# Performance work log

Measured on AMD Instinct MI355X. Metric: run time of the kernel, lower is better.

## Reference

```python
import jax, jax.numpy as jnp
import numpy as np

CAPSULES = 64
CAPSULE_DIM = 32
ROUTINGS = 3
EPS = 1e-7  # K.epsilon()


def setup_inputs() -> dict:
    key = jax.random.key(0)
    k1, k2 = jax.random.split(key)
    inputs = jax.random.normal(k1, (32, 2048, 16), dtype=jnp.float32)
    # W: (capsules, input_capsules, capsule_dim, input_capsule_dim), glorot-ish scale
    W = jax.random.normal(k2, (CAPSULES, 2048, CAPSULE_DIM, 16), dtype=jnp.float32) * 0.05
    return {"inputs": inputs, "W": W}


def squash(s):
    # s: [..., capsule_dim]
    s_norm = jnp.sum(jnp.square(s), axis=-1, keepdims=True)
    scale = s_norm / (1.0 + s_norm) / jnp.sqrt(s_norm + EPS)
    return s * scale


def reference(inputs, W):
    # inputs: [b, i, j] (batch, input_capsules, input_capsule_dim)
    # W:      [c, i, d, j] (capsules, input_capsules, capsule_dim, input_capsule_dim)
    # u_hat = batched predictions: [b, c, i, d]
    u_hat = jnp.einsum('bij,cidj->bcid', inputs, W)
    B = inputs.shape[0]
    b = jnp.zeros((B, CAPSULES, u_hat.shape[2]), dtype=u_hat.dtype)
    v = None
    for r in range(ROUTINGS):
        c = jax.nn.softmax(b, axis=1)              # softmax over capsules axis
        s = jnp.einsum('bci,bcid->bcd', c, u_hat)  # weighted sum over input capsules
        v = squash(s)                              # [b, c, d]
        # Original updates b for r > 0; the update at the final iteration has no
        # effect on the output, so it is skipped for efficiency (identical math).
        if 0 < r < ROUTINGS - 1:
            b = b + jnp.einsum('bcd,bcid->bci', v, u_hat)
    return v
```

## Files before the change

### kernel.cpp

```cpp
#include <hip/hip_runtime.h>
#include <math.h>

#define B_   32
#define I_   2048
#define J_   16
#define C_   64
#define D_   32
#define CD_  2048
#define W_CSTR (I_*D_*J_)
#define W_ISTR (D_*J_)
#define X_BSTR (I_*J_)
#define EPS_ 1e-7f

typedef _Float16 half8 __attribute__((ext_vector_type(8)));
typedef float    f32x16 __attribute__((ext_vector_type(16)));


__device__ __forceinline__ half8 wfrag_from_f32(const float* __restrict__ W,
                                                int c, int i, int l) {
  const float* wp = W + (size_t)c*W_CSTR + (size_t)i*W_ISTR
                      + (size_t)(l & 31)*J_ + ((l >> 5) << 3);
  float4 a = *(const float4*)wp;
  float4 b = *(const float4*)(wp + 4);
  half8 h;
  h[0]=(_Float16)a.x; h[1]=(_Float16)a.y; h[2]=(_Float16)a.z; h[3]=(_Float16)a.w;
  h[4]=(_Float16)b.x; h[5]=(_Float16)b.y; h[6]=(_Float16)b.z; h[7]=(_Float16)b.w;
  return h;
}

__global__ __launch_bounds__(256) void k_xpack(const float* __restrict__ x,
                                               half8* __restrict__ xh) {
  const int tg = blockIdx.x*256 + threadIdx.x;
  const int i = tg >> 6, l = tg & 63;
  const int b = l & 31, jb = (l >> 5) << 3;
  const float* xp = x + (size_t)b*X_BSTR + (size_t)i*J_ + jb;
  float4 a = *(const float4*)xp;
  float4 bb = *(const float4*)(xp + 4);
  half8 h;
  h[0]=(_Float16)a.x;  h[1]=(_Float16)a.y;  h[2]=(_Float16)a.z;  h[3]=(_Float16)a.w;
  h[4]=(_Float16)bb.x; h[5]=(_Float16)bb.y; h[6]=(_Float16)bb.z; h[7]=(_Float16)bb.w;
  xh[tg] = h;
}

template<bool WRITE_WB>
__global__ __launch_bounds__(512, 4) void k_passA(const float* __restrict__ W,
                                                  const half8* __restrict__ xh,
                                                  float* __restrict__ part,
                                                  _Float16* __restrict__ WB) {
  const int t = threadIdx.x, l = t & 63, w = t >> 6;
  const int ic = blockIdx.x, c = blockIdx.y*8 + w;
  const int b = l & 31, h4 = (l >> 5)*4;
  f32x16 acc = {};
  #pragma unroll 4
  for (int ii = 0; ii < 32; ii++) {
    const int i = ic*32 + ii;
    half8 wf = wfrag_from_f32(W, c, i, l);
    half8 xf = xh[(size_t)i*64 + l];
    if (WRITE_WB)
      *(half8*)(WB + ((size_t)c*I_ + i)*512 + (size_t)l*8) = wf;
    acc = __builtin_amdgcn_mfma_f32_32x32x16_f16(wf, xf, acc, 0, 0, 0);
  }
  #pragma unroll
  for (int r = 0; r < 16; r++) {
    const int dr = (r & 3) + 8*(r >> 2) + h4;
    part[(size_t)ic*(B_*CD_) + ((size_t)c*32 + dr)*32 + b] = acc[r];
  }
}

template<bool TOUT>
__global__ __launch_bounds__(1024) void k_redsquash(const float* __restrict__ part,
                                                    float* __restrict__ outp,
                                                    float scale) {
  __shared__ float SN[1024];
  const int c = blockIdx.x, t = threadIdx.x;
  const int d = t >> 5, b = t & 31;
  float s = 0.f;
  #pragma unroll 8
  for (int ch = 0; ch < 64; ch++) s += part[(size_t)ch*(B_*CD_) + c*1024 + t];
  s *= scale;
  SN[t] = s*s;
  __syncthreads();
  #pragma unroll
  for (int st = 16; st >= 1; st >>= 1) {
    if (d < st) SN[t] += SN[t + st*32];
    __syncthreads();
  }
  const float sn = SN[b];
  const float sc = sn / ((1.f + sn) * sqrtf(sn + EPS_));
  const float val = s*sc;
  if (TOUT) outp[(size_t)b*CD_ + c*32 + d] = val;
  else      outp[(size_t)c*1024 + t] = val;
}

template<bool USE_WB>
__global__ __launch_bounds__(512, 4) void k_blogit(const float* __restrict__ W,
                                                   const _Float16* __restrict__ WB,
                                                   const half8* __restrict__ xh,
                                                   const float* __restrict__ v1,
                                                   float* __restrict__ b1) {
  const int t = threadIdx.x, l = t & 63, w = t >> 6;
  const int ic = blockIdx.x, c = blockIdx.y*8 + w;
  const int b = l & 31, h4 = (l >> 5)*4;

  float v1r[16];
  #pragma unroll
  for (int r = 0; r < 16; r++) {
    const int dr = (r & 3) + 8*(r >> 2) + h4;
    v1r[r] = v1[(size_t)c*1024 + dr*32 + b];
  }

  #pragma unroll 4
  for (int ii = 0; ii < 32; ii++) {
    const int i = ic*32 + ii;
    half8 wf = USE_WB ? *(const half8*)(WB + ((size_t)c*I_ + i)*512 + (size_t)l*8)
                      : wfrag_from_f32(W, c, i, l);
    half8 xf = xh[(size_t)i*64 + l];
    f32x16 z = {};
    f32x16 u = __builtin_amdgcn_mfma_f32_32x32x16_f16(wf, xf, z, 0, 0, 0);
    float y = 0.f;
    #pragma unroll
    for (int r = 0; r < 16; r++) y += u[r]*v1r[r];
    y += __shfl_xor(y, 32);
    if (l < 32)
      b1[((size_t)i*64 + c)*32 + b] = y;
  }
}

__global__ __launch_bounds__(256) void k_softmaxT(const float* __restrict__ b1,
                                                  float* __restrict__ c2) {
  __shared__ float ST[2048];
  __shared__ float PM[256], PS[256];
  const int i = blockIdx.x, t = threadIdx.x;
  const float* src = b1 + (size_t)i*2048;
  *(float4*)(ST + t*8)     = *(const float4*)(src + t*8);
  *(float4*)(ST + t*8 + 4) = *(const float4*)(src + t*8 + 4);
  __syncthreads();
  const int b = t & 31, ck = t >> 5;
  float m = -1e30f;
  #pragma unroll
  for (int cc = 0; cc < 8; cc++) m = fmaxf(m, ST[(ck*8 + cc)*32 + b]);
  PM[t] = m;
  __syncthreads();
  #pragma unroll
  for (int k = 0; k < 8; k++) m = fmaxf(m, PM[k*32 + b]);
  float s = 0.f;
  #pragma unroll
  for (int cc = 0; cc < 8; cc++) {
    const int idx = (ck*8 + cc)*32 + b;
    const float e = __expf(ST[idx] - m);
    s += e;
    ST[idx] = e;
  }
  PS[t] = s;
  __syncthreads();
  s = 0.f;
  #pragma unroll
  for (int k = 0; k < 8; k++) s += PS[k*32 + b];
  const float inv = 1.f / s;
  float* dst = c2 + (size_t)i*2048;
  #pragma unroll
  for (int cc = 0; cc < 8; cc++) {
    const int idx = (ck*8 + cc)*32 + b;
    dst[idx] = ST[idx] * inv;
  }
}

template<bool USE_WB>
__global__ __launch_bounds__(512, 4) void k_passB2(const float* __restrict__ W,
                                                   const _Float16* __restrict__ WB,
                                                   const half8* __restrict__ xh,
                                                   const float* __restrict__ c2,
                                                   float* __restrict__ part) {
  const int t = threadIdx.x, l = t & 63, w = t >> 6;
  const int ic = blockIdx.x, c = blockIdx.y*8 + w;
  const int b = l & 31, h4 = (l >> 5)*4;
  f32x16 s2 = {};
  #pragma unroll 4
  for (int ii = 0; ii < 32; ii++) {
    const int i = ic*32 + ii;
    half8 wf = USE_WB ? *(const half8*)(WB + ((size_t)c*I_ + i)*512 + (size_t)l*8)
                      : wfrag_from_f32(W, c, i, l);
    half8 xf = xh[(size_t)i*64 + l];
    f32x16 z = {};
    f32x16 u = __builtin_amdgcn_mfma_f32_32x32x16_f16(wf, xf, z, 0, 0, 0);
    const float cv = c2[((size_t)i*64 + c)*32 + b];
    #pragma unroll
    for (int r = 0; r < 16; r++) s2[r] += cv*u[r];
  }
  #pragma unroll
  for (int r = 0; r < 16; r++) {
    const int dr = (r & 3) + 8*(r >> 2) + h4;
    part[(size_t)ic*(B_*CD_) + ((size_t)c*32 + dr)*32 + b] = s2[r];
  }
}

extern "C" void kernel_launch(void* const* d_in, const int* in_sizes, int n_in,
                              void* d_out, int out_size, void* d_ws, size_t ws_size,
                              hipStream_t stream) {
  (void)in_sizes; (void)n_in; (void)out_size;
  const float* x = (const float*)d_in[0];
  const float* W = (const float*)d_in[1];
  float* out = (float*)d_out;

  const size_t MiB = 1024*1024;
  char* ws = (char*)d_ws;
  const bool big = ws_size >= 163*MiB;

  _Float16* WB; float *part, *b1, *c2, *xhp, *v1;
  if (big) {
    WB    = (_Float16*)(ws);
    part  = (float*)(ws + 128*MiB);
    b1    = part;
    c2    = (float*)(ws + 144*MiB);
    xhp   = (float*)(ws + 160*MiB);
    v1    = (float*)(ws + 162*MiB);
  } else {
    WB    = nullptr;
    part  = (float*)(ws);
    b1    = part;
    c2    = (float*)(ws + 16*MiB);
    xhp   = (float*)(ws + 32*MiB);
    v1    = (float*)(ws + 34*MiB);
  }
  half8* xh = (half8*)xhp;

  k_xpack<<<512, 256, 0, stream>>>(x, xh);
  if (big) k_passA<true ><<<dim3(64, 8), 512, 0, stream>>>(W, xh, part, WB);
  else     k_passA<false><<<dim3(64, 8), 512, 0, stream>>>(W, xh, part, WB);
  k_redsquash<false><<<64, 1024, 0, stream>>>(part, v1, 1.f/64.f);
  if (big) k_blogit<true ><<<dim3(64, 8), 512, 0, stream>>>(W, WB, xh, v1, b1);
  else     k_blogit<false><<<dim3(64, 8), 512, 0, stream>>>(W, WB, xh, v1, b1);
  k_softmaxT<<<2048, 256, 0, stream>>>(b1, c2);
  if (big) k_passB2<true ><<<dim3(64, 8), 512, 0, stream>>>(W, WB, xh, c2, part);
  else     k_passB2<false><<<dim3(64, 8), 512, 0, stream>>>(W, WB, xh, c2, part);
  k_redsquash<true><<<64, 1024, 0, stream>>>(part, out, 1.f);
}
```

Measured before the change: 456.3 us.

## Stage W/x fragments via async global-to-LDS ring buffers and split reductions

Adds a separate W fp32-to-fp16 packing kernel in place of packing inside the first pass. The three MFMA passes now load x fragments into LDS once per block and stream W fragments through a 3-deep per-wave LDS ring using global_load_lds with explicit vmcnt waits, so memory latency overlaps with MFMA work. The logit kernel buffers its outputs and writes them after the loop, the c2 weights are preloaded, and the 64-way partial reduction is split into two kernels to raise parallelism. In exchange it adds kernel launches, a larger workspace requirement and hand-written waitcnt sequencing that depends on instruction ordering.

```diff
diff --git a/kernel.cpp b/kernel.cpp
--- a/kernel.cpp
+++ b/kernel.cpp
@@ -1,5 +1,6 @@
 #include <hip/hip_runtime.h>
 #include <math.h>
+#include <stdint.h>
 
 #define B_   32
 #define I_   2048
@@ -15,6 +16,18 @@
 typedef _Float16 half8 __attribute__((ext_vector_type(8)));
 typedef float    f32x16 __attribute__((ext_vector_type(16)));
 
+
+__device__ __forceinline__ void glds16(const void* g, void* l) {
+  __builtin_amdgcn_global_load_lds(
+      (const __attribute__((address_space(1))) void*)g,
+      (__attribute__((address_space(3))) void*)l, 16, 0, 0);
+}
+
+#define WAITK(k) do {                                                      \
+    if ((k) < 30)       asm volatile("s_waitcnt vmcnt(2)" ::: "memory");   \
+    else if ((k) == 30) asm volatile("s_waitcnt vmcnt(1)" ::: "memory");   \
+    else                asm volatile("s_waitcnt vmcnt(0)" ::: "memory");   \
+  } while (0)
 
 __device__ __forceinline__ half8 wfrag_from_f32(const float* __restrict__ W,
                                                 int c, int i, int l) {
@@ -42,22 +55,63 @@
   xh[tg] = h;
 }
 
-template<bool WRITE_WB>
-__global__ __launch_bounds__(512, 4) void k_passA(const float* __restrict__ W,
+__global__ __launch_bounds__(256) void k_wpack(const float* __restrict__ W,
+                                               half8* __restrict__ WBv) {
+  const int t0 = blockIdx.x*256 + threadIdx.x;
+  #pragma unroll
+  for (int it = 0; it < 4; it++) {
+    const int g = t0 + it*2097152;
+    const int l = g & 63;
+    const size_t tile = (size_t)(g >> 6);
+    const float* wp = W + tile*512 + (size_t)(l & 31)*16 + ((l >> 5) << 3);
+    float4 a  = *(const float4*)wp;
+    float4 bb = *(const float4*)(wp + 4);
+    half8 h;
+    h[0]=(_Float16)a.x;  h[1]=(_Float16)a.y;  h[2]=(_Float16)a.z;  h[3]=(_Float16)a.w;
+    h[4]=(_Float16)bb.x; h[5]=(_Float16)bb.y; h[6]=(_Float16)bb.z; h[7]=(_Float16)bb.w;
+    WBv[g] = h;
+  }
+}
+
+template<bool USE_WB>
+__global__ __launch_bounds__(512, 4) void k_mfmaA(const float* __restrict__ W,
+                                                  const _Float16* __restrict__ WB,
                                                   const half8* __restrict__ xh,
-                                                  float* __restrict__ part,
-                                                  _Float16* __restrict__ WB) {
+                                                  float* __restrict__ part) {
+  __shared__ __align__(16) char XH[32*1024];
+  __shared__ __align__(16) char RING[8*3*1024];
   const int t = threadIdx.x, l = t & 63, w = t >> 6;
   const int ic = blockIdx.x, c = blockIdx.y*8 + w;
   const int b = l & 31, h4 = (l >> 5)*4;
+
+  const char* xsrc = (const char*)xh + (size_t)ic*32*1024;
+  #pragma unroll
+  for (int q = 0; q < 4; q++) {
+    const int k = w*4 + q;
+    glds16(xsrc + (size_t)k*1024 + (size_t)l*16, XH + k*1024);
+  }
+  char* ring = RING + w*3*1024;
+  const char* wsrc = (const char*)WB + ((size_t)c*I_ + (size_t)ic*32)*1024;
+  if (USE_WB) {
+    glds16(wsrc + (size_t)l*16, ring);
+    glds16(wsrc + 1024 + (size_t)l*16, ring + 1024);
+  }
+  asm volatile("s_waitcnt vmcnt(0)" ::: "memory");
+  __syncthreads();
+
   f32x16 acc = {};
-  #pragma unroll 4
-  for (int ii = 0; ii < 32; ii++) {
-    const int i = ic*32 + ii;
-    half8 wf = wfrag_from_f32(W, c, i, l);
-    half8 xf = xh[(size_t)i*64 + l];
-    if (WRITE_WB)
-      *(half8*)(WB + ((size_t)c*I_ + i)*512 + (size_t)l*8) = wf;
+  #pragma unroll
+  for (int k = 0; k < 32; k++) {
+    half8 wf;
+    if (USE_WB) {
+      if (k + 2 < 32)
+        glds16(wsrc + (size_t)(k+2)*1024 + (size_t)l*16, ring + ((k+2)%3)*1024);
+      WAITK(k);
+      wf = *(const half8*)(ring + (k%3)*1024 + l*16);
+    } else {
+      wf = wfrag_from_f32(W, c, ic*32 + k, l);
+    }
+    half8 xf = *(const half8*)(XH + k*1024 + l*16);
     acc = __builtin_amdgcn_mfma_f32_32x32x16_f16(wf, xf, acc, 0, 0, 0);
   }
   #pragma unroll
@@ -67,16 +121,26 @@
   }
 }
 
+__global__ __launch_bounds__(1024) void k_red1(const float* __restrict__ part,
+                                               float* __restrict__ red) {
+  const int c = blockIdx.x & 63, q = blockIdx.x >> 6, t = threadIdx.x;
+  float s = 0.f;
+  #pragma unroll
+  for (int ch = 0; ch < 16; ch++)
+    s += part[(size_t)(q*16 + ch)*(B_*CD_) + c*1024 + t];
+  red[((size_t)q*64 + c)*1024 + t] = s;
+}
+
 template<bool TOUT>
-__global__ __launch_bounds__(1024) void k_redsquash(const float* __restrict__ part,
-                                                    float* __restrict__ outp,
-                                                    float scale) {
+__global__ __launch_bounds__(1024) void k_red2(const float* __restrict__ red,
+                                               float* __restrict__ outp,
+                                               float scale) {
   __shared__ float SN[1024];
   const int c = blockIdx.x, t = threadIdx.x;
   const int d = t >> 5, b = t & 31;
   float s = 0.f;
-  #pragma unroll 8
-  for (int ch = 0; ch < 64; ch++) s += part[(size_t)ch*(B_*CD_) + c*1024 + t];
+  #pragma unroll
+  for (int q = 0; q < 4; q++) s += red[((size_t)q*64 + c)*1024 + t];
   s *= scale;
   SN[t] = s*s;
   __syncthreads();
@@ -93,11 +157,13 @@
 }
 
 template<bool USE_WB>
-__global__ __launch_bounds__(512, 4) void k_blogit(const float* __restrict__ W,
-                                                   const _Float16* __restrict__ WB,
-                                                   const half8* __restrict__ xh,
-                                                   const float* __restrict__ v1,
-                                                   float* __restrict__ b1) {
+__global__ __launch_bounds__(512, 4) void k_blogit2(const float* __restrict__ W,
+                                                    const _Float16* __restrict__ WB,
+                                                    const half8* __restrict__ xh,
+                                                    const float* __restrict__ v1,
+                                                    float* __restrict__ b1) {
+  __shared__ __align__(16) char XH[32*1024];
+  __shared__ __align__(16) char RING[8*3*1024];
   const int t = threadIdx.x, l = t & 63, w = t >> 6;
   const int ic = blockIdx.x, c = blockIdx.y*8 + w;
   const int b = l & 31, h4 = (l >> 5)*4;
@@ -109,20 +175,46 @@
     v1r[r] = v1[(size_t)c*1024 + dr*32 + b];
   }
 
-  #pragma unroll 4
-  for (int ii = 0; ii < 32; ii++) {
-    const int i = ic*32 + ii;
-    half8 wf = USE_WB ? *(const half8*)(WB + ((size_t)c*I_ + i)*512 + (size_t)l*8)
-                      : wfrag_from_f32(W, c, i, l);
-    half8 xf = xh[(size_t)i*64 + l];
+  const char* xsrc = (const char*)xh + (size_t)ic*32*1024;
+  #pragma unroll
+  for (int q = 0; q < 4; q++) {
+    const int k = w*4 + q;
+    glds16(xsrc + (size_t)k*1024 + (size_t)l*16, XH + k*1024);
+  }
+  char* ring = RING + w*3*1024;
+  const char* wsrc = (const char*)WB + ((size_t)c*I_ + (size_t)ic*32)*1024;
+  if (USE_WB) {
+    glds16(wsrc + (size_t)l*16, ring);
+    glds16(wsrc + 1024 + (size_t)l*16, ring + 1024);
+  }
+  asm volatile("s_waitcnt vmcnt(0)" ::: "memory");
+  __syncthreads();
+
+  float yv[32];
+  #pragma unroll
+  for (int k = 0; k < 32; k++) {
+    half8 wf;
+    if (USE_WB) {
+      if (k + 2 < 32)
+        glds16(wsrc + (size_t)(k+2)*1024 + (size_t)l*16, ring + ((k+2)%3)*1024);
+      WAITK(k);
+      wf = *(const half8*)(ring + (k%3)*1024 + l*16);
+    } else {
+      wf = wfrag_from_f32(W, c, ic*32 + k, l);
+    }
+    half8 xf = *(const half8*)(XH + k*1024 + l*16);
     f32x16 z = {};
     f32x16 u = __builtin_amdgcn_mfma_f32_32x32x16_f16(wf, xf, z, 0, 0, 0);
     float y = 0.f;
     #pragma unroll
     for (int r = 0; r < 16; r++) y += u[r]*v1r[r];
     y += __shfl_xor(y, 32);
-    if (l < 32)
-      b1[((size_t)i*64 + c)*32 + b] = y;
+    yv[k] = y;
+  }
+  if (l < 32) {
+    #pragma unroll
+    for (int k = 0; k < 32; k++)
+      b1[((size_t)(ic*32 + k)*64 + c)*32 + b] = yv[k];
   }
 }
 
@@ -166,26 +258,54 @@
 }
 
 template<bool USE_WB>
-__global__ __launch_bounds__(512, 4) void k_passB2(const float* __restrict__ W,
+__global__ __launch_bounds__(512, 4) void k_mfmaB2(const float* __restrict__ W,
                                                    const _Float16* __restrict__ WB,
                                                    const half8* __restrict__ xh,
                                                    const float* __restrict__ c2,
                                                    float* __restrict__ part) {
+  __shared__ __align__(16) char XH[32*1024];
+  __shared__ __align__(16) char RING[8*3*1024];
   const int t = threadIdx.x, l = t & 63, w = t >> 6;
   const int ic = blockIdx.x, c = blockIdx.y*8 + w;
   const int b = l & 31, h4 = (l >> 5)*4;
+
+  float cv[32];
+  #pragma unroll
+  for (int k = 0; k < 32; k++)
+    cv[k] = c2[((size_t)(ic*32 + k)*64 + c)*32 + b];
+
+  const char* xsrc = (const char*)xh + (size_t)ic*32*1024;
+  #pragma unroll
+  for (int q = 0; q < 4; q++) {
+    const int k = w*4 + q;
+    glds16(xsrc + (size_t)k*1024 + (size_t)l*16, XH + k*1024);
+  }
+  char* ring = RING + w*3*1024;
+  const char* wsrc = (const char*)WB + ((size_t)c*I_ + (size_t)ic*32)*1024;
+  if (USE_WB) {
+    glds16(wsrc + (size_t)l*16, ring);
+    glds16(wsrc + 1024 + (size_t)l*16, ring + 1024);
+  }
+  asm volatile("s_waitcnt vmcnt(0)" ::: "memory");
+  __syncthreads();
+
   f32x16 s2 = {};
-  #pragma unroll 4
-  for (int ii = 0; ii < 32; ii++) {
-    const int i = ic*32 + ii;
-    half8 wf = USE_WB ? *(const half8*)(WB + ((size_t)c*I_ + i)*512 + (size_t)l*8)
-                      : wfrag_from_f32(W, c, i, l);
-    half8 xf = xh[(size_t)i*64 + l];
+  #pragma unroll
+  for (int k = 0; k < 32; k++) {
+    half8 wf;
+    if (USE_WB) {
+      if (k + 2 < 32)
+        glds16(wsrc + (size_t)(k+2)*1024 + (size_t)l*16, ring + ((k+2)%3)*1024);
+      WAITK(k);
+      wf = *(const half8*)(ring + (k%3)*1024 + l*16);
+    } else {
+      wf = wfrag_from_f32(W, c, ic*32 + k, l);
+    }
+    half8 xf = *(const half8*)(XH + k*1024 + l*16);
     f32x16 z = {};
     f32x16 u = __builtin_amdgcn_mfma_f32_32x32x16_f16(wf, xf, z, 0, 0, 0);
-    const float cv = c2[((size_t)i*64 + c)*32 + b];
     #pragma unroll
-    for (int r = 0; r < 16; r++) s2[r] += cv*u[r];
+    for (int r = 0; r < 16; r++) s2[r] += cv[k]*u[r];
   }
   #pragma unroll
   for (int r = 0; r < 16; r++) {
@@ -204,9 +324,9 @@
 
   const size_t MiB = 1024*1024;
   char* ws = (char*)d_ws;
-  const bool big = ws_size >= 163*MiB;
-
-  _Float16* WB; float *part, *b1, *c2, *xhp, *v1;
+  const bool big = ws_size >= 164*MiB;
+
+  _Float16* WB; float *part, *b1, *c2, *xhp, *v1, *red;
   if (big) {
     WB    = (_Float16*)(ws);
     part  = (float*)(ws + 128*MiB);
@@ -214,6 +334,7 @@
     c2    = (float*)(ws + 144*MiB);
     xhp   = (float*)(ws + 160*MiB);
     v1    = (float*)(ws + 162*MiB);
+    red   = (float*)(ws + 163*MiB);
   } else {
     WB    = nullptr;
     part  = (float*)(ws);
@@ -221,17 +342,24 @@
     c2    = (float*)(ws + 16*MiB);
     xhp   = (float*)(ws + 32*MiB);
     v1    = (float*)(ws + 34*MiB);
+    red   = (float*)(ws + 35*MiB);
   }
   half8* xh = (half8*)xhp;
 
   k_xpack<<<512, 256, 0, stream>>>(x, xh);
-  if (big) k_passA<true ><<<dim3(64, 8), 512, 0, stream>>>(W, xh, part, WB);
-  else     k_passA<false><<<dim3(64, 8), 512, 0, stream>>>(W, xh, part, WB);
-  k_redsquash<false><<<64, 1024, 0, stream>>>(part, v1, 1.f/64.f);
-  if (big) k_blogit<true ><<<dim3(64, 8), 512, 0, stream>>>(W, WB, xh, v1, b1);
-  else     k_blogit<false><<<dim3(64, 8), 512, 0, stream>>>(W, WB, xh, v1, b1);
+  if (big) {
+    k_wpack<<<8192, 256, 0, stream>>>(W, (half8*)WB);
+    k_mfmaA<true ><<<dim3(64, 8), 512, 0, stream>>>(W, WB, xh, part);
+  } else {
+    k_mfmaA<false><<<dim3(64, 8), 512, 0, stream>>>(W, WB, xh, part);
+  }
+  k_red1<<<256, 1024, 0, stream>>>(part, red);
+  k_red2<false><<<64, 1024, 0, stream>>>(red, v1, 1.f/64.f);
+  if (big) k_blogit2<true ><<<dim3(64, 8), 512, 0, stream>>>(W, WB, xh, v1, b1);
+  else     k_blogit2<false><<<dim3(64, 8), 512, 0, stream>>>(W, WB, xh, v1, b1);
   k_softmaxT<<<2048, 256, 0, stream>>>(b1, c2);
-  if (big) k_passB2<true ><<<dim3(64, 8), 512, 0, stream>>>(W, WB, xh, c2, part);
-  else     k_passB2<false><<<dim3(64, 8), 512, 0, stream>>>(W, WB, xh, c2, part);
-  k_redsquash<true><<<64, 1024, 0, stream>>>(part, out, 1.f);
-}
+  if (big) k_mfmaB2<true ><<<dim3(64, 8), 512, 0, stream>>>(W, WB, xh, c2, part);
+  else     k_mfmaB2<false><<<dim3(64, 8), 512, 0, stream>>>(W, WB, xh, c2, part);
+  k_red1<<<256, 1024, 0, stream>>>(part, red);
+  k_red2<true><<<64, 1024, 0, stream>>>(red, out, 1.f);
+}
```

Result: slower. 477.2 us (+4.6%).

## Fuse routing logits with softmax and split partial reduction into two stages

Applied to the files above, without the earlier changes.

The logit kernel now has each block handle 8 input capsules across all 64 output capsules, keeping the logits in shared memory and applying the softmax over capsules in place. This removes the separate softmax kernel and the global round trip of the logit buffer. The 64-way partial-sum reduction is split into a 256-block first stage and a 64-block squash stage to use more of the GPU. The costs are one extra launch per reduction, a 64KB shared-memory footprint in the fused kernel that lowers occupancy, and a softmax done serially by 256 threads.

```diff
diff --git a/kernel.cpp b/kernel.cpp
--- a/kernel.cpp
+++ b/kernel.cpp
@@ -1,5 +1,6 @@
 #include <hip/hip_runtime.h>
 #include <math.h>
+#include <stdint.h>
 
 #define B_   32
 #define I_   2048
@@ -67,16 +68,26 @@
   }
 }
 
+__global__ __launch_bounds__(1024) void k_red1(const float* __restrict__ part,
+                                               float* __restrict__ red) {
+  const int c = blockIdx.x & 63, q = blockIdx.x >> 6, t = threadIdx.x;
+  float s = 0.f;
+  #pragma unroll
+  for (int ch = 0; ch < 16; ch++)
+    s += part[(size_t)(q*16 + ch)*(B_*CD_) + c*1024 + t];
+  red[((size_t)q*64 + c)*1024 + t] = s;
+}
+
 template<bool TOUT>
-__global__ __launch_bounds__(1024) void k_redsquash(const float* __restrict__ part,
-                                                    float* __restrict__ outp,
-                                                    float scale) {
+__global__ __launch_bounds__(1024) void k_red2(const float* __restrict__ red,
+                                               float* __restrict__ outp,
+                                               float scale) {
   __shared__ float SN[1024];
   const int c = blockIdx.x, t = threadIdx.x;
   const int d = t >> 5, b = t & 31;
   float s = 0.f;
-  #pragma unroll 8
-  for (int ch = 0; ch < 64; ch++) s += part[(size_t)ch*(B_*CD_) + c*1024 + t];
+  #pragma unroll
+  for (int q = 0; q < 4; q++) s += red[((size_t)q*64 + c)*1024 + t];
   s *= scale;
   SN[t] = s*s;
   __syncthreads();
@@ -93,76 +104,67 @@
 }
 
 template<bool USE_WB>
-__global__ __launch_bounds__(512, 4) void k_blogit(const float* __restrict__ W,
-                                                   const _Float16* __restrict__ WB,
-                                                   const half8* __restrict__ xh,
-                                                   const float* __restrict__ v1,
-                                                   float* __restrict__ b1) {
+__global__ __launch_bounds__(512, 4) void k_blogitF(const float* __restrict__ W,
+                                                    const _Float16* __restrict__ WB,
+                                                    const half8* __restrict__ xh,
+                                                    const float* __restrict__ v1,
+                                                    float* __restrict__ c2) {
+  __shared__ float Y[8][64][32];
   const int t = threadIdx.x, l = t & 63, w = t >> 6;
-  const int ic = blockIdx.x, c = blockIdx.y*8 + w;
+  const int i0 = blockIdx.x*8;
   const int b = l & 31, h4 = (l >> 5)*4;
 
-  float v1r[16];
-  #pragma unroll
-  for (int r = 0; r < 16; r++) {
-    const int dr = (r & 3) + 8*(r >> 2) + h4;
-    v1r[r] = v1[(size_t)c*1024 + dr*32 + b];
-  }
-
-  #pragma unroll 4
-  for (int ii = 0; ii < 32; ii++) {
-    const int i = ic*32 + ii;
-    half8 wf = USE_WB ? *(const half8*)(WB + ((size_t)c*I_ + i)*512 + (size_t)l*8)
-                      : wfrag_from_f32(W, c, i, l);
-    half8 xf = xh[(size_t)i*64 + l];
-    f32x16 z = {};
-    f32x16 u = __builtin_amdgcn_mfma_f32_32x32x16_f16(wf, xf, z, 0, 0, 0);
-    float y = 0.f;
-    #pragma unroll
-    for (int r = 0; r < 16; r++) y += u[r]*v1r[r];
-    y += __shfl_xor(y, 32);
-    if (l < 32)
-      b1[((size_t)i*64 + c)*32 + b] = y;
-  }
-}
-
-__global__ __launch_bounds__(256) void k_softmaxT(const float* __restrict__ b1,
-                                                  float* __restrict__ c2) {
-  __shared__ float ST[2048];
-  __shared__ float PM[256], PS[256];
-  const int i = blockIdx.x, t = threadIdx.x;
-  const float* src = b1 + (size_t)i*2048;
-  *(float4*)(ST + t*8)     = *(const float4*)(src + t*8);
-  *(float4*)(ST + t*8 + 4) = *(const float4*)(src + t*8 + 4);
+  half8 xf[8];
+  #pragma unroll
+  for (int ii = 0; ii < 8; ii++) xf[ii] = xh[(size_t)(i0 + ii)*64 + l];
+
+  #pragma unroll 1
+  for (int cc = 0; cc < 8; cc++) {
+    const int c = cc*8 + w;
+    float v1r[16];
+    #pragma unroll
+    for (int r = 0; r < 16; r++) {
+      const int dr = (r & 3) + 8*(r >> 2) + h4;
+      v1r[r] = v1[(size_t)c*1024 + dr*32 + b];
+    }
+    #pragma unroll
+    for (int ii = 0; ii < 8; ii++) {
+      half8 wf = USE_WB
+        ? *(const half8*)(WB + ((size_t)c*I_ + i0 + ii)*512 + (size_t)l*8)
+        : wfrag_from_f32(W, c, i0 + ii, l);
+      f32x16 z = {};
+      f32x16 u = __builtin_amdgcn_mfma_f32_32x32x16_f16(wf, xf[ii], z, 0, 0, 0);
+      float y = 0.f;
+      #pragma unroll
+      for (int r = 0; r < 16; r++) y += u[r]*v1r[r];
+      y += __shfl_xor(y, 32);
+      if (l < 32) Y[ii][c][b] = y;
+    }
+  }
   __syncthreads();
-  const int b = t & 31, ck = t >> 5;
-  float m = -1e30f;
-  #pragma unroll
-  for (int cc = 0; cc < 8; cc++) m = fmaxf(m, ST[(ck*8 + cc)*32 + b]);
-  PM[t] = m;
+
+  if (t < 256) {
+    const int ii = t >> 5, bb = t & 31;
+    float m = -1e30f;
+    #pragma unroll
+    for (int c = 0; c < 64; c++) m = fmaxf(m, Y[ii][c][bb]);
+    float s = 0.f;
+    #pragma unroll
+    for (int c = 0; c < 64; c++) {
+      const float e = __expf(Y[ii][c][bb] - m);
+      s += e;
+      Y[ii][c][bb] = e;
+    }
+    const float inv = 1.f / s;
+    #pragma unroll
+    for (int c = 0; c < 64; c++) Y[ii][c][bb] *= inv;
+  }
   __syncthreads();
-  #pragma unroll
-  for (int k = 0; k < 8; k++) m = fmaxf(m, PM[k*32 + b]);
-  float s = 0.f;
-  #pragma unroll
-  for (int cc = 0; cc < 8; cc++) {
-    const int idx = (ck*8 + cc)*32 + b;
-    const float e = __expf(ST[idx] - m);
-    s += e;
-    ST[idx] = e;
-  }
-  PS[t] = s;
-  __syncthreads();
-  s = 0.f;
-  #pragma unroll
-  for (int k = 0; k < 8; k++) s += PS[k*32 + b];
-  const float inv = 1.f / s;
-  float* dst = c2 + (size_t)i*2048;
-  #pragma unroll
-  for (int cc = 0; cc < 8; cc++) {
-    const int idx = (ck*8 + cc)*32 + b;
-    dst[idx] = ST[idx] * inv;
-  }
+
+  float4* dst = (float4*)(c2 + (size_t)i0*2048);
+  const float4* srcv = (const float4*)&Y[0][0][0];
+  #pragma unroll
+  for (int q = 0; q < 8; q++) dst[q*512 + t] = srcv[q*512 + t];
 }
 
 template<bool USE_WB>
@@ -204,34 +206,35 @@
 
   const size_t MiB = 1024*1024;
   char* ws = (char*)d_ws;
-  const bool big = ws_size >= 163*MiB;
-
-  _Float16* WB; float *part, *b1, *c2, *xhp, *v1;
+  const bool big = ws_size >= 164*MiB;
+
+  _Float16* WB; float *part, *c2, *xhp, *v1, *red;
   if (big) {
     WB    = (_Float16*)(ws);
     part  = (float*)(ws + 128*MiB);
-    b1    = part;
     c2    = (float*)(ws + 144*MiB);
     xhp   = (float*)(ws + 160*MiB);
     v1    = (float*)(ws + 162*MiB);
+    red   = (float*)(ws + 163*MiB);
   } else {
     WB    = nullptr;
     part  = (float*)(ws);
-    b1    = part;
     c2    = (float*)(ws + 16*MiB);
     xhp   = (float*)(ws + 32*MiB);
     v1    = (float*)(ws + 34*MiB);
+    red   = (float*)(ws + 35*MiB);
   }
   half8* xh = (half8*)xhp;
 
   k_xpack<<<512, 256, 0, stream>>>(x, xh);
   if (big) k_passA<true ><<<dim3(64, 8), 512, 0, stream>>>(W, xh, part, WB);
   else     k_passA<false><<<dim3(64, 8), 512, 0, stream>>>(W, xh, part, WB);
-  k_redsquash<false><<<64, 1024, 0, stream>>>(part, v1, 1.f/64.f);
-  if (big) k_blogit<true ><<<dim3(64, 8), 512, 0, stream>>>(W, WB, xh, v1, b1);
-  else     k_blogit<false><<<dim3(64, 8), 512, 0, stream>>>(W, WB, xh, v1, b1);
-  k_softmaxT<<<2048, 256, 0, stream>>>(b1, c2);
+  k_red1<<<256, 1024, 0, stream>>>(part, red);
+  k_red2<false><<<64, 1024, 0, stream>>>(red, v1, 1.f/64.f);
+  if (big) k_blogitF<true ><<<256, 512, 0, stream>>>(W, WB, xh, v1, c2);
+  else     k_blogitF<false><<<256, 512, 0, stream>>>(W, WB, xh, v1, c2);
   if (big) k_passB2<true ><<<dim3(64, 8), 512, 0, stream>>>(W, WB, xh, c2, part);
   else     k_passB2<false><<<dim3(64, 8), 512, 0, stream>>>(W, WB, xh, c2, part);
-  k_redsquash<true><<<64, 1024, 0, stream>>>(part, out, 1.f);
-}
+  k_red1<<<256, 1024, 0, stream>>>(part, red);
+  k_red2<true><<<64, 1024, 0, stream>>>(red, out, 1.f);
+}
```

Result: slower. 470.9 us (+3.2%).
